# Kernel tuning notes

Hardware: AMD Instinct MI355X
Metric: run time of the kernel (lower is better)

## Reference

```python
import jax, jax.numpy as jnp
from jax import lax
import numpy as np

CHANNELS = 16
THRESH = 0.1
UPDATE_RATE = 0.25


def _sobel_kernel():
    ident = np.array([[0., 0., 0.], [0., 1., 0.], [0., 0., 0.]], np.float32)
    sx = np.array([[-1., 0., 1.], [-2., 0., 2.], [-1., 0., 1.]], np.float32)
    sy = sx.T
    k = np.stack([ident, sx, sy])[:, None, :, :]          # [3,1,3,3]
    k = np.tile(k, (CHANNELS, 1, 1, 1))                   # [48,1,3,3] (torch repeat order)
    return jnp.asarray(k)


def _perceive(x, w_sobel):
    # circular pad then depthwise grouped conv (groups=CHANNELS, 3 filters per group)
    xp = jnp.pad(x, ((0, 0), (0, 0), (1, 1), (1, 1)), mode='wrap')
    return lax.conv_general_dilated(
        xp, w_sobel, window_strides=(1, 1), padding='VALID',
        dimension_numbers=('NCHW', 'OIHW', 'NCHW'),
        feature_group_count=CHANNELS)                     # [B,48,H,W]


def _alive_mask(x):
    alpha = x[:, 3:4]                                     # [B,1,H,W]
    p = jnp.pad(alpha, ((0, 0), (0, 0), (1, 1), (1, 1)), mode='wrap')
    m = lax.reduce_window(p, -jnp.inf, lax.max, (1, 1, 3, 3), (1, 1, 1, 1), 'VALID')
    return (m > THRESH).astype(x.dtype)


def _mlp(y, w1, b1, w2, b2, w3):
    h = jax.nn.relu(jnp.einsum('bchw,oc->bohw', y, w1) + b1[None, :, None, None])
    h = jax.nn.relu(jnp.einsum('bchw,oc->bohw', h, w2) + b2[None, :, None, None])
    return jnp.einsum('bchw,oc->bohw', h, w3)             # [B,16,H,W], no bias


def setup_inputs() -> dict:
    key = jax.random.key(0)
    ks = jax.random.split(key, 7)
    B, H, W, steps = 8, 256, 256, 2
    s = 0.1
    return {
        'x': jax.random.uniform(ks[0], (B, CHANNELS, H, W), jnp.float32),
        'w1': jax.random.normal(ks[1], (64, 48), jnp.float32) * s,
        'b1': jax.random.normal(ks[2], (64,), jnp.float32) * s,
        'w2': jax.random.normal(ks[3], (64, 64), jnp.float32) * s,
        'b2': jax.random.normal(ks[4], (64,), jnp.float32) * s,
        'w3': jax.random.normal(ks[5], (CHANNELS, 64), jnp.float32) * s,
        'update_masks': jax.random.uniform(ks[6], (steps, B, 1, H, W), jnp.float32),
        'steps': steps,
    }


def reference(x, w1, b1, w2, b2, w3, update_masks, steps):
    w_sobel = _sobel_kernel()
    for i in range(steps):
        pre = _alive_mask(x)
        y = _mlp(_perceive(x, w_sobel), w1, b1, w2, b2, w3)
        um = (update_masks[i] < UPDATE_RATE).astype(x.dtype)
        x = x + y * um
        post = _alive_mask(x)
        x = x * (pre * post)
    return x
```

## Files before the change

kernel.cpp:

```cpp
#include <hip/hip_runtime.h>
#include <hip/hip_bf16.h>

#define NB 8
#define NC 16
#define NH 256
#define NW 256
#define ALIVE_THRESH 0.1f
#define UPDATE_RATE 0.25f

typedef __attribute__((ext_vector_type(8))) short bf16x8;
typedef __attribute__((ext_vector_type(4))) float f32x4;
typedef unsigned short ushort_t;

#define MFMA16(a, b, c) __builtin_amdgcn_mfma_f32_16x16x32_bf16((a), (b), (c), 0, 0, 0)

static __device__ __forceinline__ unsigned short f2bf(float f) {
    __hip_bfloat16 h = __float2bfloat16(f);
    return __builtin_bit_cast(unsigned short, h);
}
static __device__ __forceinline__ float bf2f(unsigned short b) {
    union { unsigned u; float f; } x; x.u = ((unsigned)b) << 16; return x.f;
}
static __device__ __forceinline__ unsigned pack2(float lo, float hi) {
    return (unsigned)f2bf(lo) | ((unsigned)f2bf(hi) << 16);
}
static __device__ __forceinline__ float bfbits(unsigned w, int hi) {
    return bf2f((unsigned short)(hi ? (w >> 16) : (w & 0xffffu)));
}

static __device__ __forceinline__ int ybyte(int px, int g) {
    return px * 128 + ((g ^ (px & 7)) << 4);
}

struct WFrags {
    bf16x8 a1[8];
    bf16x8 a2[8];
    bf16x8 a3[2];
    f32x4  b2v[4];
};

static __device__ __forceinline__ WFrags load_wfrags(
    const int4* __restrict__ wf, const float* __restrict__ b2, int lane)
{
    WFrags w;
    #pragma unroll
    for (int f = 0; f < 8; ++f)
        w.a1[f] = __builtin_bit_cast(bf16x8, wf[f * 64 + lane]);
    #pragma unroll
    for (int f = 0; f < 8; ++f)
        w.a2[f] = __builtin_bit_cast(bf16x8, wf[(8 + f) * 64 + lane]);
    w.a3[0] = __builtin_bit_cast(bf16x8, wf[16 * 64 + lane]);
    w.a3[1] = __builtin_bit_cast(bf16x8, wf[17 * 64 + lane]);
    const int lq = lane >> 4;
    #pragma unroll
    for (int mt = 0; mt < 4; ++mt)
        w.b2v[mt] = *(const f32x4*)(b2 + mt * 16 + lq * 4);
    return w;
}

__global__ void prep_weights(const float* __restrict__ w1, const float* __restrict__ b1,
                             const float* __restrict__ w2, const float* __restrict__ w3,
                             int4* __restrict__ wf)
{
    const int f = blockIdx.x, l = threadIdx.x;
    const int lq = l >> 4, ln = l & 15;
    union { unsigned short us[8]; int4 v; } u;
    if (f < 8) {
        const int mt = f >> 1, ks = f & 1, m = mt * 16 + ln;
        #pragma unroll
        for (int j = 0; j < 8; ++j) {
            const int k = ks * 32 + lq * 8 + j;
            float v = (k < 48) ? w1[m * 48 + k] : ((k == 48) ? b1[m] : 0.0f);
            u.us[j] = f2bf(v);
        }
    } else if (f < 16) {
        const int ff = f - 8, mt = ff >> 1, ks = ff & 1, m = mt * 16 + ln;
        #pragma unroll
        for (int j = 0; j < 8; ++j)
            u.us[j] = f2bf(w2[m * 64 + (ks * 32 + lq * 8 + j)]);
    } else {
        const int ks = f - 16, m = ln;
        #pragma unroll
        for (int j = 0; j < 8; ++j)
            u.us[j] = f2bf(w3[m * 64 + (ks * 32 + lq * 8 + j)]);
    }
    wf[f * 64 + l] = u.v;
}

static __device__ __forceinline__ void combine_store(
    char* yb, unsigned* sd, int t, const float* mreg, const float* dreg)
{
    __syncthreads();
    const int tm = (t - 1) & 255, tp = (t + 1) & 255;
    unsigned yp[24];
    {
        unsigned short ys[48];
        #pragma unroll
        for (int c = 0; c < NC; ++c) {
            unsigned L = sd[c * NW + tm], R = sd[c * NW + tp];
            float sl = bfbits(L, 0), dl = bfbits(L, 1);
            float sr = bfbits(R, 0), dr = bfbits(R, 1);
            ys[3 * c + 0] = f2bf(mreg[c]);
            ys[3 * c + 1] = f2bf(sr - sl);
            ys[3 * c + 2] = f2bf(dl + 2.0f * dreg[c] + dr);
        }
        #pragma unroll
        for (int i = 0; i < 24; ++i)
            yp[i] = (unsigned)ys[2 * i] | ((unsigned)ys[2 * i + 1] << 16);
    }
    __syncthreads();

    #pragma unroll
    for (int g = 0; g < 6; ++g) {
        union { unsigned w[4]; int4 v; } pk;
        pk.w[0] = yp[4 * g]; pk.w[1] = yp[4 * g + 1];
        pk.w[2] = yp[4 * g + 2]; pk.w[3] = yp[4 * g + 3];
        *(int4*)(yb + ybyte(t, g)) = pk.v;
    }
    { int4 br; br.x = 0x3F80; br.y = 0; br.z = 0; br.w = 0;
      *(int4*)(yb + ybyte(t, 6)) = br; }
    { int4 zz; zz.x = zz.y = zz.z = zz.w = 0;
      *(int4*)(yb + ybyte(t, 7)) = zz; }
}

template<typename ResF, typename OutF>
static __device__ __forceinline__ void mlp_gemm(
    char* yb, int lane, int px0, const WFrags& wfr, float um_own,
    ResF getres, OutF putout)
{
    const int lq = lane >> 4, ln = lane & 15;

    float umv[4];
    #pragma unroll
    for (int nt = 0; nt < 4; ++nt)
        umv[nt] = (__shfl(um_own, nt * 16 + ln) < UPDATE_RATE) ? 1.0f : 0.0f;

    #pragma unroll
    for (int nt = 0; nt < 4; ++nt) {
        const int px = px0 + nt * 16 + ln;
        bf16x8 bb0 = *(const bf16x8*)(yb + ybyte(px, lq));
        bf16x8 bb1 = *(const bf16x8*)(yb + ybyte(px, 4 + lq));
        #pragma unroll
        for (int mt = 0; mt < 4; ++mt) {
            f32x4 z = {0.f, 0.f, 0.f, 0.f};
            z = MFMA16(wfr.a1[2 * mt],     bb0, z);
            z = MFMA16(wfr.a1[2 * mt + 1], bb1, z);
            union { unsigned w[2]; uint2 v; } pk;
            pk.w[0] = pack2(fmaxf(z[0], 0.f), fmaxf(z[1], 0.f));
            pk.w[1] = pack2(fmaxf(z[2], 0.f), fmaxf(z[3], 0.f));
            *(uint2*)(yb + ybyte(px, 2 * mt + (lq >> 1)) + (lq & 1) * 8) = pk.v;
        }
    }

    #pragma unroll
    for (int nt = 0; nt < 4; ++nt) {
        const int px = px0 + nt * 16 + ln;
        bf16x8 bb0 = *(const bf16x8*)(yb + ybyte(px, lq));
        bf16x8 bb1 = *(const bf16x8*)(yb + ybyte(px, 4 + lq));
        #pragma unroll
        for (int mt = 0; mt < 4; ++mt) {
            f32x4 z = {0.f, 0.f, 0.f, 0.f};
            z = MFMA16(wfr.a2[2 * mt],     bb0, z);
            z = MFMA16(wfr.a2[2 * mt + 1], bb1, z);
            z = z + wfr.b2v[mt];
            union { unsigned w[2]; uint2 v; } pk;
            pk.w[0] = pack2(fmaxf(z[0], 0.f), fmaxf(z[1], 0.f));
            pk.w[1] = pack2(fmaxf(z[2], 0.f), fmaxf(z[3], 0.f));
            *(uint2*)(yb + ybyte(px, 2 * mt + (lq >> 1)) + (lq & 1) * 8) = pk.v;
        }
    }

    #pragma unroll
    for (int nt = 0; nt < 4; ++nt) {
        const int px = px0 + nt * 16 + ln;
        bf16x8 bb0 = *(const bf16x8*)(yb + ybyte(px, lq));
        bf16x8 bb1 = *(const bf16x8*)(yb + ybyte(px, 4 + lq));
        f32x4 z = {0.f, 0.f, 0.f, 0.f};
        z = MFMA16(wfr.a3[0], bb0, z);
        z = MFMA16(wfr.a3[1], bb1, z);
        f32x4 res = getres(px, lq);
        #pragma unroll
        for (int r = 0; r < 4; ++r)
            putout(px, lq, r, res[r] + z[r] * umv[nt]);
    }
}

__global__ __launch_bounds__(256, 3) void nca_first(
    const float* __restrict__ x,
    const float* __restrict__ um,
    const int4*  __restrict__ wf,
    const float* __restrict__ b2,
    ushort_t* __restrict__ xout,
    unsigned char* __restrict__ preb_out)
{
    __shared__ char smem[256 * 128];
    char*     yb = smem;
    unsigned* sd = (unsigned*)smem;

    const int t = threadIdx.x, bx = blockIdx.x;
    const int h = ((bx & 7) << 5) | (bx >> 3);
    const int b = blockIdx.y;
    const int hm = (h - 1) & 255, hp = (h + 1) & 255;
    const size_t cs = (size_t)NH * NW;
    const size_t base = (size_t)b * NC * cs;
    const size_t prow = (size_t)b * NH;
    const int lane = t & 63;

    const WFrags wfr = load_wfrags(wf, b2, lane);
    const float um_own = um[(prow + h) * NW + t];

    {
        const float* a3p = x + base + 3 * cs;
        float mx = -1e30f;
        #pragma unroll
        for (int r = 0; r < 3; ++r) {
            const float* rp = a3p + (size_t)((h - 1 + r) & 255) * NW;
            #pragma unroll
            for (int d = 0; d < 3; ++d)
                mx = fmaxf(mx, rp[(t - 1 + d) & 255]);
        }
        preb_out[(prow + h) * NW + t] = (mx > ALIVE_THRESH) ? 1 : 0;
    }

    float mreg[NC], dreg[NC];
    #pragma unroll
    for (int c = 0; c < NC; ++c) {
        const float* xc = x + base + (size_t)c * cs;
        float top = xc[(size_t)hm * NW + t];
        float mid = xc[(size_t)h  * NW + t];
        float bot = xc[(size_t)hp * NW + t];
        sd[c * NW + t] = pack2(top + 2.0f * mid + bot, bot - top);
        mreg[c] = mid; dreg[c] = bot - top;
    }

    combine_store(yb, sd, t, mreg, dreg);

    const int wv = t >> 6;

    auto getres = [&](int px, int lq) -> f32x4 {
        f32x4 r;
        #pragma unroll
        for (int i = 0; i < 4; ++i)
            r[i] = x[base + (size_t)(lq * 4 + i) * cs + (size_t)h * NW + px];
        return r;
    };
    auto putout = [&](int px, int lq, int r, float v) {
        xout[base + (size_t)(lq * 4 + r) * cs + (size_t)h * NW + px] = f2bf(v);
    };
    mlp_gemm(yb, lane, wv * 64, wfr, um_own, getres, putout);
}

__global__ __launch_bounds__(256, 3) void nca_step(
    const ushort_t* __restrict__ xin,
    const unsigned char* __restrict__ preb_in,
    const float* __restrict__ um,
    const int4*  __restrict__ wf,
    const float* __restrict__ b2,
    ushort_t* __restrict__ xout,
    unsigned char* __restrict__ preb_out)
{
    __shared__ char smem[256 * 128];
    char*     yb = smem;
    unsigned* sd = (unsigned*)smem;

    const int t = threadIdx.x, bx = blockIdx.x;
    const int h = ((bx & 7) << 5) | (bx >> 3);
    const int b = blockIdx.y;
    const int hm = (h - 1) & 255, hp = (h + 1) & 255;
    const size_t cs = (size_t)NH * NW;
    const size_t base = (size_t)b * NC * cs;
    const size_t prow = (size_t)b * NH;
    const int lane = t & 63;

    const WFrags wfr = load_wfrags(wf, b2, lane);
    const float um_own = um[(prow + h) * NW + t];

    float a[5][5];
    {
        const ushort_t* a3p = xin + base + 3 * cs;
        #pragma unroll
        for (int j = 0; j < 5; ++j) {
            const ushort_t* rp = a3p + (size_t)((h - 2 + j) & 255) * NW;
            #pragma unroll
            for (int d = 0; d < 5; ++d)
                a[j][d] = bf2f(rp[(t - 2 + d) & 255]);
        }
    }

    float m3x3[3][3];
    #pragma unroll
    for (int r = 0; r < 3; ++r) {
        float cm[5];
        #pragma unroll
        for (int d = 0; d < 5; ++d)
            cm[d] = fmaxf(fmaxf(a[r][d], a[r + 1][d]), a[r + 2][d]);
        #pragma unroll
        for (int dd = 0; dd < 3; ++dd) {
            float post = fmaxf(fmaxf(cm[dd], cm[dd + 1]), cm[dd + 2]);
            const int hh = (h - 1 + r) & 255, uu = (t - 1 + dd) & 255;
            unsigned char p = preb_in[(prow + hh) * NW + uu];
            m3x3[r][dd] = (post > ALIVE_THRESH && p) ? 1.0f : 0.0f;
        }
    }

    {
        float pm = 0.0f;
        #pragma unroll
        for (int r = 0; r < 3; ++r)
            #pragma unroll
            for (int dd = 0; dd < 3; ++dd)
                pm = fmaxf(pm, a[1 + r][1 + dd] * m3x3[r][dd]);
        preb_out[(prow + h) * NW + t] = (pm > ALIVE_THRESH) ? 1 : 0;
    }

    const float m0 = m3x3[0][1], m1 = m3x3[1][1], m2 = m3x3[2][1];

    float mreg[NC], dreg[NC];
    #pragma unroll
    for (int c = 0; c < NC; ++c) {
        float top, mid, bot;
        if (c == 3) { top = a[1][2] * m0; mid = a[2][2] * m1; bot = a[3][2] * m2; }
        else {
            const ushort_t* xc = xin + base + (size_t)c * cs;
            top = bf2f(xc[(size_t)hm * NW + t]) * m0;
            mid = bf2f(xc[(size_t)h  * NW + t]) * m1;
            bot = bf2f(xc[(size_t)hp * NW + t]) * m2;
        }
        sd[c * NW + t] = pack2(top + 2.0f * mid + bot, bot - top);
        mreg[c] = mid; dreg[c] = bot - top;
    }

    combine_store(yb, sd, t, mreg, dreg);

    const int wv = t >> 6;

    auto getres = [&](int px, int lq) -> f32x4 {
        const float mm = __shfl(m1, px & 63);
        f32x4 r;
        #pragma unroll
        for (int i = 0; i < 4; ++i)
            r[i] = bf2f(xin[base + (size_t)(lq * 4 + i) * cs + (size_t)h * NW + px]) * mm;
        return r;
    };
    auto putout = [&](int px, int lq, int r, float v) {
        xout[base + (size_t)(lq * 4 + r) * cs + (size_t)h * NW + px] = f2bf(v);
    };
    mlp_gemm(yb, lane, wv * 64, wfr, um_own, getres, putout);
}

__global__ __launch_bounds__(256) void nca_final(
    const ushort_t* __restrict__ xin,
    const unsigned char* __restrict__ preb,
    float* __restrict__ xout)
{
    const int t = threadIdx.x, bx = blockIdx.x;
    const int b = blockIdx.y;
    const int h = (bx << 2) | (t >> 6);
    const int px0 = (t & 63) << 2;
    const size_t cs = (size_t)NH * NW;
    const size_t base = (size_t)b * NC * cs;
    const size_t prow = (size_t)b * NH;

    const ushort_t* a3p = xin + base + 3 * cs;
    float m0 = -1e30f, m1 = -1e30f, m2 = -1e30f, m3 = -1e30f;
    #pragma unroll
    for (int r = 0; r < 3; ++r) {
        const ushort_t* rp = a3p + (size_t)((h - 1 + r) & 255) * NW;
        uint2 mid = *(const uint2*)(rp + px0);
        float v0 = bfbits(mid.x, 0), v1 = bfbits(mid.x, 1);
        float v2 = bfbits(mid.y, 0), v3 = bfbits(mid.y, 1);
        float lm = bf2f(rp[(px0 - 1) & 255]);
        float rm = bf2f(rp[(px0 + 4) & 255]);
        m0 = fmaxf(m0, fmaxf(fmaxf(lm, v0), v1));
        m1 = fmaxf(m1, fmaxf(fmaxf(v0, v1), v2));
        m2 = fmaxf(m2, fmaxf(fmaxf(v1, v2), v3));
        m3 = fmaxf(m3, fmaxf(fmaxf(v2, v3), rm));
    }
    const size_t pix = (prow + h) * NW + px0;
    const unsigned pr4 = *(const unsigned*)(preb + pix);
    const float f0 = (m0 > ALIVE_THRESH && (pr4 & 0x000000FFu)) ? 1.0f : 0.0f;
    const float f1 = (m1 > ALIVE_THRESH && (pr4 & 0x0000FF00u)) ? 1.0f : 0.0f;
    const float f2 = (m2 > ALIVE_THRESH && (pr4 & 0x00FF0000u)) ? 1.0f : 0.0f;
    const float f3 = (m3 > ALIVE_THRESH && (pr4 & 0xFF000000u)) ? 1.0f : 0.0f;

    #pragma unroll
    for (int c = 0; c < NC; ++c) {
        const size_t o = base + (size_t)c * cs + (size_t)h * NW + px0;
        uint2 s = *(const uint2*)(xin + o);
        float4 v;
        v.x = bfbits(s.x, 0) * f0;
        v.y = bfbits(s.x, 1) * f1;
        v.z = bfbits(s.y, 0) * f2;
        v.w = bfbits(s.y, 1) * f3;
        *(float4*)(xout + o) = v;
    }
}

extern "C" void kernel_launch(void* const* d_in, const int* in_sizes, int n_in,
                              void* d_out, int out_size, void* d_ws, size_t ws_size,
                              hipStream_t stream) {
    const float* x  = (const float*)d_in[0];
    const float* w1 = (const float*)d_in[1];
    const float* b1 = (const float*)d_in[2];
    const float* w2 = (const float*)d_in[3];
    const float* b2 = (const float*)d_in[4];
    const float* w3 = (const float*)d_in[5];
    const float* um = (const float*)d_in[6];
    const int steps = in_sizes[6] / (NB * NH * NW);

    const size_t npix  = (size_t)NB * NH * NW;
    const size_t nelem = (size_t)NB * NC * NH * NW;

    ushort_t* bfA        = (ushort_t*)d_ws;
    ushort_t* bfB        = bfA + nelem;
    unsigned char* prebA = (unsigned char*)(bfB + nelem);
    unsigned char* prebB = prebA + npix;
    int4* wf             = (int4*)(prebB + npix);
    float* xout          = (float*)d_out;

    prep_weights<<<18, 64, 0, stream>>>(w1, b1, w2, w3, wf);

    dim3 grd(NH, NB);
    dim3 grdF(NH / 4, NB);

    const ushort_t* cur = bfA;
    unsigned char* preb_last = prebA;

    for (int i = 0; i < steps; ++i) {
        const float* um_i = um + (size_t)i * npix;
        ushort_t* bfo      = (i % 2 == 0) ? bfA : bfB;
        unsigned char* po  = (i % 2 == 0) ? prebA : prebB;
        unsigned char* pin = (i % 2 == 0) ? prebB : prebA;

        if (i == 0)
            nca_first<<<grd, 256, 0, stream>>>(x, um_i, wf, b2, bfo, po);
        else
            nca_step<<<grd, 256, 0, stream>>>(cur, pin, um_i, wf, b2, bfo, po);
        cur = bfo;
        preb_last = po;
    }

    nca_final<<<grdF, 256, 0, stream>>>(cur, preb_last, xout);
}
```

Measured before the change: 63.47 us.

## Process two rows per block and load MLP weight fragments per layer

Each block now handles two consecutive image rows in a loop, with the grid halved to match, so block launch and setup costs are spread over more work. Weight fragments are no longer held in registers for the whole kernel; each layer's A fragments and bias are loaded just before that layer's MFMA loop, which shortens register live ranges. With the lower register pressure, launch bounds are raised from 3 to 4 blocks per CU. The cost is repeated weight reloads from cache on every row and an extra __syncthreads between rows, with less row-level parallelism in the grid.

```diff
diff --git a/kernel.cpp b/kernel.cpp
--- a/kernel.cpp
+++ b/kernel.cpp
@@ -7,6 +7,7 @@
 #define NW 256
 #define ALIVE_THRESH 0.1f
 #define UPDATE_RATE 0.25f
+#define ROWS 2
 
 typedef __attribute__((ext_vector_type(8))) short bf16x8;
 typedef __attribute__((ext_vector_type(4))) float f32x4;
@@ -30,32 +31,6 @@
 
 static __device__ __forceinline__ int ybyte(int px, int g) {
     return px * 128 + ((g ^ (px & 7)) << 4);
-}
-
-struct WFrags {
-    bf16x8 a1[8];
-    bf16x8 a2[8];
-    bf16x8 a3[2];
-    f32x4  b2v[4];
-};
-
-static __device__ __forceinline__ WFrags load_wfrags(
-    const int4* __restrict__ wf, const float* __restrict__ b2, int lane)
-{
-    WFrags w;
-    #pragma unroll
-    for (int f = 0; f < 8; ++f)
-        w.a1[f] = __builtin_bit_cast(bf16x8, wf[f * 64 + lane]);
-    #pragma unroll
-    for (int f = 0; f < 8; ++f)
-        w.a2[f] = __builtin_bit_cast(bf16x8, wf[(8 + f) * 64 + lane]);
-    w.a3[0] = __builtin_bit_cast(bf16x8, wf[16 * 64 + lane]);
-    w.a3[1] = __builtin_bit_cast(bf16x8, wf[17 * 64 + lane]);
-    const int lq = lane >> 4;
-    #pragma unroll
-    for (int mt = 0; mt < 4; ++mt)
-        w.b2v[mt] = *(const f32x4*)(b2 + mt * 16 + lq * 4);
-    return w;
 }
 
 __global__ void prep_weights(const float* __restrict__ w1, const float* __restrict__ b1,
@@ -125,8 +100,9 @@
 
 template<typename ResF, typename OutF>
 static __device__ __forceinline__ void mlp_gemm(
-    char* yb, int lane, int px0, const WFrags& wfr, float um_own,
-    ResF getres, OutF putout)
+    char* yb, int lane, int px0,
+    const int4* __restrict__ wf, const float* __restrict__ b2,
+    float um_own, ResF getres, OutF putout)
 {
     const int lq = lane >> 4, ln = lane & 15;
 
@@ -134,6 +110,11 @@
     #pragma unroll
     for (int nt = 0; nt < 4; ++nt)
         umv[nt] = (__shfl(um_own, nt * 16 + ln) < UPDATE_RATE) ? 1.0f : 0.0f;
+
+    bf16x8 a1f[8];
+    #pragma unroll
+    for (int f = 0; f < 8; ++f)
+        a1f[f] = __builtin_bit_cast(bf16x8, wf[f * 64 + lane]);
 
     #pragma unroll
     for (int nt = 0; nt < 4; ++nt) {
@@ -143,8 +124,8 @@
         #pragma unroll
         for (int mt = 0; mt < 4; ++mt) {
             f32x4 z = {0.f, 0.f, 0.f, 0.f};
-            z = MFMA16(wfr.a1[2 * mt],     bb0, z);
-            z = MFMA16(wfr.a1[2 * mt + 1], bb1, z);
+            z = MFMA16(a1f[2 * mt],     bb0, z);
+            z = MFMA16(a1f[2 * mt + 1], bb1, z);
             union { unsigned w[2]; uint2 v; } pk;
             pk.w[0] = pack2(fmaxf(z[0], 0.f), fmaxf(z[1], 0.f));
             pk.w[1] = pack2(fmaxf(z[2], 0.f), fmaxf(z[3], 0.f));
@@ -152,6 +133,15 @@
         }
     }
 
+    bf16x8 a2f[8];
+    #pragma unroll
+    for (int f = 0; f < 8; ++f)
+        a2f[f] = __builtin_bit_cast(bf16x8, wf[(8 + f) * 64 + lane]);
+    f32x4 b2v[4];
+    #pragma unroll
+    for (int mt = 0; mt < 4; ++mt)
+        b2v[mt] = *(const f32x4*)(b2 + mt * 16 + lq * 4);
+
     #pragma unroll
     for (int nt = 0; nt < 4; ++nt) {
         const int px = px0 + nt * 16 + ln;
@@ -160,15 +150,18 @@
         #pragma unroll
         for (int mt = 0; mt < 4; ++mt) {
             f32x4 z = {0.f, 0.f, 0.f, 0.f};
-            z = MFMA16(wfr.a2[2 * mt],     bb0, z);
-            z = MFMA16(wfr.a2[2 * mt + 1], bb1, z);
-            z = z + wfr.b2v[mt];
+            z = MFMA16(a2f[2 * mt],     bb0, z);
+            z = MFMA16(a2f[2 * mt + 1], bb1, z);
+            z = z + b2v[mt];
             union { unsigned w[2]; uint2 v; } pk;
             pk.w[0] = pack2(fmaxf(z[0], 0.f), fmaxf(z[1], 0.f));
             pk.w[1] = pack2(fmaxf(z[2], 0.f), fmaxf(z[3], 0.f));
             *(uint2*)(yb + ybyte(px, 2 * mt + (lq >> 1)) + (lq & 1) * 8) = pk.v;
         }
     }
+
+    bf16x8 a3f0 = __builtin_bit_cast(bf16x8, wf[16 * 64 + lane]);
+    bf16x8 a3f1 = __builtin_bit_cast(bf16x8, wf[17 * 64 + lane]);
 
     #pragma unroll
     for (int nt = 0; nt < 4; ++nt) {
@@ -176,8 +169,8 @@
         bf16x8 bb0 = *(const bf16x8*)(yb + ybyte(px, lq));
         bf16x8 bb1 = *(const bf16x8*)(yb + ybyte(px, 4 + lq));
         f32x4 z = {0.f, 0.f, 0.f, 0.f};
-        z = MFMA16(wfr.a3[0], bb0, z);
-        z = MFMA16(wfr.a3[1], bb1, z);
+        z = MFMA16(a3f0, bb0, z);
+        z = MFMA16(a3f1, bb1, z);
         f32x4 res = getres(px, lq);
         #pragma unroll
         for (int r = 0; r < 4; ++r)
@@ -185,7 +178,7 @@
     }
 }
 
-__global__ __launch_bounds__(256, 3) void nca_first(
+__global__ __launch_bounds__(256, 4) void nca_first(
     const float* __restrict__ x,
     const float* __restrict__ um,
     const int4*  __restrict__ wf,
@@ -198,59 +191,62 @@
     unsigned* sd = (unsigned*)smem;
 
     const int t = threadIdx.x, bx = blockIdx.x;
-    const int h = ((bx & 7) << 5) | (bx >> 3);
+    const int h0 = ((((bx & 7) << 4) | (bx >> 3)) << 1);
     const int b = blockIdx.y;
-    const int hm = (h - 1) & 255, hp = (h + 1) & 255;
     const size_t cs = (size_t)NH * NW;
     const size_t base = (size_t)b * NC * cs;
     const size_t prow = (size_t)b * NH;
-    const int lane = t & 63;
-
-    const WFrags wfr = load_wfrags(wf, b2, lane);
-    const float um_own = um[(prow + h) * NW + t];
-
-    {
-        const float* a3p = x + base + 3 * cs;
-        float mx = -1e30f;
-        #pragma unroll
-        for (int r = 0; r < 3; ++r) {
-            const float* rp = a3p + (size_t)((h - 1 + r) & 255) * NW;
-            #pragma unroll
-            for (int d = 0; d < 3; ++d)
-                mx = fmaxf(mx, rp[(t - 1 + d) & 255]);
-        }
-        preb_out[(prow + h) * NW + t] = (mx > ALIVE_THRESH) ? 1 : 0;
-    }
-
-    float mreg[NC], dreg[NC];
-    #pragma unroll
-    for (int c = 0; c < NC; ++c) {
-        const float* xc = x + base + (size_t)c * cs;
-        float top = xc[(size_t)hm * NW + t];
-        float mid = xc[(size_t)h  * NW + t];
-        float bot = xc[(size_t)hp * NW + t];
-        sd[c * NW + t] = pack2(top + 2.0f * mid + bot, bot - top);
-        mreg[c] = mid; dreg[c] = bot - top;
-    }
-
-    combine_store(yb, sd, t, mreg, dreg);
-
-    const int wv = t >> 6;
-
-    auto getres = [&](int px, int lq) -> f32x4 {
-        f32x4 r;
-        #pragma unroll
-        for (int i = 0; i < 4; ++i)
-            r[i] = x[base + (size_t)(lq * 4 + i) * cs + (size_t)h * NW + px];
-        return r;
-    };
-    auto putout = [&](int px, int lq, int r, float v) {
-        xout[base + (size_t)(lq * 4 + r) * cs + (size_t)h * NW + px] = f2bf(v);
-    };
-    mlp_gemm(yb, lane, wv * 64, wfr, um_own, getres, putout);
-}
-
-__global__ __launch_bounds__(256, 3) void nca_step(
+    const int lane = t & 63, wv = t >> 6;
+
+    #pragma unroll
+    for (int rr = 0; rr < ROWS; ++rr) {
+        if (rr) __syncthreads();
+        const int h = h0 + rr;
+        const int hm = (h - 1) & 255, hp = (h + 1) & 255;
+
+        const float um_own = um[(prow + h) * NW + t];
+
+        {
+            const float* a3p = x + base + 3 * cs;
+            float mx = -1e30f;
+            #pragma unroll
+            for (int r = 0; r < 3; ++r) {
+                const float* rp = a3p + (size_t)((h - 1 + r) & 255) * NW;
+                #pragma unroll
+                for (int d = 0; d < 3; ++d)
+                    mx = fmaxf(mx, rp[(t - 1 + d) & 255]);
+            }
+            preb_out[(prow + h) * NW + t] = (mx > ALIVE_THRESH) ? 1 : 0;
+        }
+
+        float mreg[NC], dreg[NC];
+        #pragma unroll
+        for (int c = 0; c < NC; ++c) {
+            const float* xc = x + base + (size_t)c * cs;
+            float top = xc[(size_t)hm * NW + t];
+            float mid = xc[(size_t)h  * NW + t];
+            float bot = xc[(size_t)hp * NW + t];
+            sd[c * NW + t] = pack2(top + 2.0f * mid + bot, bot - top);
+            mreg[c] = mid; dreg[c] = bot - top;
+        }
+
+        combine_store(yb, sd, t, mreg, dreg);
+
+        auto getres = [&](int px, int lq) -> f32x4 {
+            f32x4 r;
+            #pragma unroll
+            for (int i = 0; i < 4; ++i)
+                r[i] = x[base + (size_t)(lq * 4 + i) * cs + (size_t)h * NW + px];
+            return r;
+        };
+        auto putout = [&](int px, int lq, int r, float v) {
+            xout[base + (size_t)(lq * 4 + r) * cs + (size_t)h * NW + px] = f2bf(v);
+        };
+        mlp_gemm(yb, lane, wv * 64, wf, b2, um_own, getres, putout);
+    }
+}
+
+__global__ __launch_bounds__(256, 4) void nca_step(
     const ushort_t* __restrict__ xin,
     const unsigned char* __restrict__ preb_in,
     const float* __restrict__ um,
@@ -264,88 +260,91 @@
     unsigned* sd = (unsigned*)smem;
 
     const int t = threadIdx.x, bx = blockIdx.x;
-    const int h = ((bx & 7) << 5) | (bx >> 3);
+    const int h0 = ((((bx & 7) << 4) | (bx >> 3)) << 1);
     const int b = blockIdx.y;
-    const int hm = (h - 1) & 255, hp = (h + 1) & 255;
     const size_t cs = (size_t)NH * NW;
     const size_t base = (size_t)b * NC * cs;
     const size_t prow = (size_t)b * NH;
-    const int lane = t & 63;
-
-    const WFrags wfr = load_wfrags(wf, b2, lane);
-    const float um_own = um[(prow + h) * NW + t];
-
-    float a[5][5];
-    {
-        const ushort_t* a3p = xin + base + 3 * cs;
-        #pragma unroll
-        for (int j = 0; j < 5; ++j) {
-            const ushort_t* rp = a3p + (size_t)((h - 2 + j) & 255) * NW;
+    const int lane = t & 63, wv = t >> 6;
+
+    #pragma unroll
+    for (int rr = 0; rr < ROWS; ++rr) {
+        if (rr) __syncthreads();
+        const int h = h0 + rr;
+        const int hm = (h - 1) & 255, hp = (h + 1) & 255;
+
+        const float um_own = um[(prow + h) * NW + t];
+
+        float a[5][5];
+        {
+            const ushort_t* a3p = xin + base + 3 * cs;
+            #pragma unroll
+            for (int j = 0; j < 5; ++j) {
+                const ushort_t* rp = a3p + (size_t)((h - 2 + j) & 255) * NW;
+                #pragma unroll
+                for (int d = 0; d < 5; ++d)
+                    a[j][d] = bf2f(rp[(t - 2 + d) & 255]);
+            }
+        }
+
+        float m3x3[3][3];
+        #pragma unroll
+        for (int r = 0; r < 3; ++r) {
+            float cm[5];
             #pragma unroll
             for (int d = 0; d < 5; ++d)
-                a[j][d] = bf2f(rp[(t - 2 + d) & 255]);
-        }
-    }
-
-    float m3x3[3][3];
-    #pragma unroll
-    for (int r = 0; r < 3; ++r) {
-        float cm[5];
-        #pragma unroll
-        for (int d = 0; d < 5; ++d)
-            cm[d] = fmaxf(fmaxf(a[r][d], a[r + 1][d]), a[r + 2][d]);
-        #pragma unroll
-        for (int dd = 0; dd < 3; ++dd) {
-            float post = fmaxf(fmaxf(cm[dd], cm[dd + 1]), cm[dd + 2]);
-            const int hh = (h - 1 + r) & 255, uu = (t - 1 + dd) & 255;
-            unsigned char p = preb_in[(prow + hh) * NW + uu];
-            m3x3[r][dd] = (post > ALIVE_THRESH && p) ? 1.0f : 0.0f;
-        }
-    }
-
-    {
-        float pm = 0.0f;
-        #pragma unroll
-        for (int r = 0; r < 3; ++r)
-            #pragma unroll
-            for (int dd = 0; dd < 3; ++dd)
-                pm = fmaxf(pm, a[1 + r][1 + dd] * m3x3[r][dd]);
-        preb_out[(prow + h) * NW + t] = (pm > ALIVE_THRESH) ? 1 : 0;
-    }
-
-    const float m0 = m3x3[0][1], m1 = m3x3[1][1], m2 = m3x3[2][1];
-
-    float mreg[NC], dreg[NC];
-    #pragma unroll
-    for (int c = 0; c < NC; ++c) {
-        float top, mid, bot;
-        if (c == 3) { top = a[1][2] * m0; mid = a[2][2] * m1; bot = a[3][2] * m2; }
-        else {
-            const ushort_t* xc = xin + base + (size_t)c * cs;
-            top = bf2f(xc[(size_t)hm * NW + t]) * m0;
-            mid = bf2f(xc[(size_t)h  * NW + t]) * m1;
-            bot = bf2f(xc[(size_t)hp * NW + t]) * m2;
-        }
-        sd[c * NW + t] = pack2(top + 2.0f * mid + bot, bot - top);
-        mreg[c] = mid; dreg[c] = bot - top;
-    }
-
-    combine_store(yb, sd, t, mreg, dreg);
-
-    const int wv = t >> 6;
-
-    auto getres = [&](int px, int lq) -> f32x4 {
-        const float mm = __shfl(m1, px & 63);
-        f32x4 r;
-        #pragma unroll
-        for (int i = 0; i < 4; ++i)
-            r[i] = bf2f(xin[base + (size_t)(lq * 4 + i) * cs + (size_t)h * NW + px]) * mm;
-        return r;
-    };
-    auto putout = [&](int px, int lq, int r, float v) {
-        xout[base + (size_t)(lq * 4 + r) * cs + (size_t)h * NW + px] = f2bf(v);
-    };
-    mlp_gemm(yb, lane, wv * 64, wfr, um_own, getres, putout);
+                cm[d] = fmaxf(fmaxf(a[r][d], a[r + 1][d]), a[r + 2][d]);
+            #pragma unroll
+            for (int dd = 0; dd < 3; ++dd) {
+                float post = fmaxf(fmaxf(cm[dd], cm[dd + 1]), cm[dd + 2]);
+                const int hh = (h - 1 + r) & 255, uu = (t - 1 + dd) & 255;
+                unsigned char p = preb_in[(prow + hh) * NW + uu];
+                m3x3[r][dd] = (post > ALIVE_THRESH && p) ? 1.0f : 0.0f;
+            }
+        }
+
+        {
+            float pm = 0.0f;
+            #pragma unroll
+            for (int r = 0; r < 3; ++r)
+                #pragma unroll
+                for (int dd = 0; dd < 3; ++dd)
+                    pm = fmaxf(pm, a[1 + r][1 + dd] * m3x3[r][dd]);
+            preb_out[(prow + h) * NW + t] = (pm > ALIVE_THRESH) ? 1 : 0;
+        }
+
+        const float m0 = m3x3[0][1], m1 = m3x3[1][1], m2 = m3x3[2][1];
+
+        float mreg[NC], dreg[NC];
+        #pragma unroll
+        for (int c = 0; c < NC; ++c) {
+            float top, mid, bot;
+            if (c == 3) { top = a[1][2] * m0; mid = a[2][2] * m1; bot = a[3][2] * m2; }
+            else {
+                const ushort_t* xc = xin + base + (size_t)c * cs;
+                top = bf2f(xc[(size_t)hm * NW + t]) * m0;
+                mid = bf2f(xc[(size_t)h  * NW + t]) * m1;
+                bot = bf2f(xc[(size_t)hp * NW + t]) * m2;
+            }
+            sd[c * NW + t] = pack2(top + 2.0f * mid + bot, bot - top);
+            mreg[c] = mid; dreg[c] = bot - top;
+        }
+
+        combine_store(yb, sd, t, mreg, dreg);
+
+        auto getres = [&](int px, int lq) -> f32x4 {
+            const float mm = __shfl(m1, px & 63);
+            f32x4 r;
+            #pragma unroll
+            for (int i = 0; i < 4; ++i)
+                r[i] = bf2f(xin[base + (size_t)(lq * 4 + i) * cs + (size_t)h * NW + px]) * mm;
+            return r;
+        };
+        auto putout = [&](int px, int lq, int r, float v) {
+            xout[base + (size_t)(lq * 4 + r) * cs + (size_t)h * NW + px] = f2bf(v);
+        };
+        mlp_gemm(yb, lane, wv * 64, wf, b2, um_own, getres, putout);
+    }
 }
 
 __global__ __launch_bounds__(256) void nca_final(
@@ -420,7 +419,7 @@
 
     prep_weights<<<18, 64, 0, stream>>>(w1, b1, w2, w3, wf);
 
-    dim3 grd(NH, NB);
+    dim3 grd(NH / ROWS, NB);
     dim3 grdF(NH / 4, NB);
 
     const ushort_t* cur = bfA;
```

Measured after the change: 75.65 us. 1.19x slower.
